# Performance work log

Hardware: AMD Instinct MI355X
Metric: run time of the kernel (lower is better)

Reference implementation:

```python
import jax, jax.numpy as jnp
import numpy as np

H = 128
N_USER, N_TXN, N_DEVICE = 200000, 400000, 100000
E = 600000


def setup_inputs() -> dict:
    key = jax.random.key(0)
    ks = jax.random.split(key, 16)
    s = 0.05
    return {
        "x_user": jax.random.normal(ks[0], (N_USER, H), jnp.float32),
        "x_txn": jax.random.normal(ks[1], (N_TXN, H), jnp.float32),
        "x_device": jax.random.normal(ks[2], (N_DEVICE, H), jnp.float32),
        "es0": jax.random.randint(ks[3], (E,), 0, N_TXN),
        "ed0": jax.random.randint(ks[4], (E,), 0, N_USER),
        "es1": jax.random.randint(ks[5], (E,), 0, N_DEVICE),
        "ed1": jax.random.randint(ks[6], (E,), 0, N_USER),
        "es2": jax.random.randint(ks[7], (E,), 0, N_USER),
        "ed2": jax.random.randint(ks[8], (E,), 0, N_USER),
        "Wl": jax.random.normal(ks[9], (3, H, H), jnp.float32) * s,
        "bl": jax.random.normal(ks[10], (3, H), jnp.float32) * s,
        "Wr": jax.random.normal(ks[11], (3, H, H), jnp.float32) * s,
        "W1": jax.random.normal(ks[12], (H, 3 * H), jnp.float32) * s,
        "b1": jax.random.normal(ks[13], (H,), jnp.float32) * s,
        "W2": jax.random.normal(ks[14], (H, H), jnp.float32) * s,
        "b2": jax.random.normal(ks[15], (H,), jnp.float32) * s,
    }


def _sage(x_src, x_dst, es, ed, wl, b, wr):
    # PyG SAGEConv (mean aggr): lin_l(mean of neighbor feats) + lin_r(x_dst)
    n_dst = x_dst.shape[0]
    msgs = x_src[es]                                   # [E, H] gather
    agg = jax.ops.segment_sum(msgs, ed, num_segments=n_dst)   # [N_dst, H]
    cnt = jax.ops.segment_sum(jnp.ones((es.shape[0],), x_src.dtype), ed,
                              num_segments=n_dst)
    mean = agg / jnp.maximum(cnt, 1.0)[:, None]
    return mean @ wl.T + b + x_dst @ wr.T


def reference(x_user, x_txn, x_device, es0, ed0, es1, ed1, es2, ed2,
              Wl, bl, Wr, W1, b1, W2, b2):
    o0 = _sage(x_txn, x_user, es0, ed0, Wl[0], bl[0], Wr[0])
    o1 = _sage(x_device, x_user, es1, ed1, Wl[1], bl[1], Wr[1])
    o2 = _sage(x_user, x_user, es2, ed2, Wl[2], bl[2], Wr[2])
    combined = jnp.concatenate([o0, o1, o2], axis=-1)  # [N_user, 3H]
    h = jax.nn.relu(combined @ W1.T + b1)
    return h @ W2.T + b2
```

## Files before the change

kernel.cpp:

```cpp
#include <hip/hip_runtime.h>

#define H 128

typedef float v2f __attribute__((ext_vector_type(2)));

__global__ __launch_bounds__(128) void precompute_kernel(
    const float* __restrict__ Wl, const float* __restrict__ bl,
    const float* __restrict__ Wr, const float* __restrict__ W1,
    const float* __restrict__ b1, const float* __restrict__ W2,
    const float* __restrict__ b2,
    float* __restrict__ Am, float* __restrict__ W2T,
    float* __restrict__ cvec, float* __restrict__ b2f)
{
  int b = blockIdx.x;
  int j = threadIdx.x;
  if (b < 512) {
    int mat = b >> 7;
    int m   = b & 127;
    float s = 0.f;
    if (mat < 3) {
      int r = mat;
      for (int i = 0; i < H; i++)
        s += Wl[r*H*H + i*H + m] * W1[j*3*H + r*H + i];
    } else {
      for (int r = 0; r < 3; r++)
        for (int i = 0; i < H; i++)
          s += Wr[r*H*H + i*H + m] * W1[j*3*H + r*H + i];
    }
    Am[mat*H*H + m*H + j] = s;
  } else if (b == 512) {
    float s = b1[j];
    for (int r = 0; r < 3; r++)
      for (int i = 0; i < H; i++)
        s += bl[r*H + i] * W1[j*3*H + r*H + i];
    cvec[j] = s;
    b2f[j]  = b2[j];
  } else {
    int m = b - 513;
    W2T[m*H + j] = W2[j*H + m];
  }
}

__global__ __launch_bounds__(256) void k_hist3(
    const int* __restrict__ ed0, const int* __restrict__ ed1,
    const int* __restrict__ ed2, int* __restrict__ cntA,
    int NU, int E0, int E1, int E2)
{
  int r = blockIdx.y;
  const int* ed = (r == 0) ? ed0 : (r == 1) ? ed1 : ed2;
  int E = (r == 0) ? E0 : (r == 1) ? E1 : E2;
  int i = blockIdx.x * 256 + threadIdx.x;
  if (i < E) atomicAdd(&cntA[(size_t)r * NU + ed[i]], 1);
}

__global__ __launch_bounds__(256) void k_scan1(
    const int* __restrict__ degA, int* __restrict__ offA,
    int* __restrict__ bsumA, int n, int nb1)
{
  int r = blockIdx.y;
  const int* deg = degA + (size_t)r * n;
  int* off1 = offA + (size_t)r * (n + 1);
  int* bsum = bsumA + (size_t)r * nb1;
  __shared__ int tmp[256];
  int i = blockIdx.x * 256 + threadIdx.x;
  int v = (i < n) ? deg[i] : 0;
  tmp[threadIdx.x] = v;
  __syncthreads();
  for (int s = 1; s < 256; s <<= 1) {
    int t = (threadIdx.x >= (unsigned)s) ? tmp[threadIdx.x - s] : 0;
    __syncthreads();
    tmp[threadIdx.x] += t;
    __syncthreads();
  }
  if (i < n) off1[i + 1] = tmp[threadIdx.x];
  if (threadIdx.x == 255) bsum[blockIdx.x] = tmp[255];
}

__global__ __launch_bounds__(256) void k_scan3c(
    int* __restrict__ offA, const int* __restrict__ bsumA,
    int* __restrict__ curA, int n, int nb1)
{
  int r = blockIdx.y;
  int* off = offA + (size_t)r * (n + 1);
  const int* bsum = bsumA + (size_t)r * nb1;
  int* cur = curA + (size_t)r * n;
  __shared__ int red[256];
  int a = 0;
  for (int i = threadIdx.x; i < blockIdx.x; i += 256) a += bsum[i];
  red[threadIdx.x] = a;
  __syncthreads();
  for (int s = 128; s > 0; s >>= 1) {
    if (threadIdx.x < (unsigned)s) red[threadIdx.x] += red[threadIdx.x + s];
    __syncthreads();
  }
  int prefix = red[0];
  int i = blockIdx.x * 256 + threadIdx.x;
  if (i < n) {
    int d = cur[i];
    int o = off[i + 1] + prefix;
    off[i + 1] = o;
    cur[i] = o - d;
  }
  if (blockIdx.x == 0 && threadIdx.x == 0) off[0] = 0;
}

__global__ __launch_bounds__(256) void k_scatter3(
    const int* __restrict__ es0, const int* __restrict__ es1,
    const int* __restrict__ es2,
    const int* __restrict__ ed0, const int* __restrict__ ed1,
    const int* __restrict__ ed2,
    int* __restrict__ curA,
    int* __restrict__ nbr0, int* __restrict__ nbr1, int* __restrict__ nbr2,
    int NU, int E0, int E1, int E2)
{
  int r = blockIdx.y;
  const int* es = (r == 0) ? es0 : (r == 1) ? es1 : es2;
  const int* ed = (r == 0) ? ed0 : (r == 1) ? ed1 : ed2;
  int* nbr = (r == 0) ? nbr0 : (r == 1) ? nbr1 : nbr2;
  int* cur = curA + (size_t)r * NU;
  int E = (r == 0) ? E0 : (r == 1) ? E1 : E2;
  int i = blockIdx.x * 256 + threadIdx.x;
  if (i < E) {
    int d = ed[i];
    int pos = atomicAdd(&cur[d], 1);
    nbr[pos] = es[i];
  }
}

__device__ __forceinline__ void mm_accum(const float* __restrict__ W,
                                         float (*xs)[130], float* wb,
                                         v2f* acc, int tid, int nA, int c)
{
  for (int mc = 0; mc < 4; mc++) {
    __syncthreads();
    {
      int m = tid >> 3;
      const float4* s4 = (const float4*)(W + (size_t)(mc * 32 + m) * H + c * 16);
      float4* dd = (float4*)(wb + c * 516 + m * 16);
      dd[0] = s4[0]; dd[1] = s4[1]; dd[2] = s4[2]; dd[3] = s4[3];
    }
    __syncthreads();
    const float* xr = &xs[nA][mc * 32];
    const float4* wq = (const float4*)(wb + c * 516);
#pragma unroll 4
    for (int m = 0; m < 32; m++) {
      float xm = xr[m];
      v2f xv; xv[0] = xm; xv[1] = xm;
      const float4* w4 = wq + m * 4;
#pragma unroll
      for (int q = 0; q < 4; q++) {
        float4 w = w4[q];
        v2f w01; w01[0] = w.x; w01[1] = w.y;
        v2f w23; w23[0] = w.z; w23[1] = w.w;
        acc[2*q]   += xv * w01;
        acc[2*q+1] += xv * w23;
      }
    }
  }
}

__global__ __launch_bounds__(256, 4) void k_fused(
    const float* __restrict__ xu, const float* __restrict__ xt,
    const float* __restrict__ xd,
    const int* __restrict__ off0, const int* __restrict__ nbr0,
    const int* __restrict__ off1, const int* __restrict__ nbr1,
    const int* __restrict__ off2, const int* __restrict__ nbr2,
    const float* __restrict__ Am, const float* __restrict__ W2T,
    const float* __restrict__ cvec, const float* __restrict__ b2f,
    float* __restrict__ out, int NU)
{
  __shared__ float xs[32][130];
  __shared__ float wb[8 * 516];
  int tid = threadIdx.x;
  int c = tid & 7, j0 = c * 16, nA = tid >> 3;
  int q = tid & 7;
  int g0 = blockIdx.x * 32;
  int g = g0 + nA;

  v2f acc[8];
  {
    const v2f* cv = (const v2f*)(cvec + j0);
#pragma unroll
    for (int qq = 0; qq < 8; qq++) acc[qq] = cv[qq];
  }

  for (int s = 0; s < 4; s++) {
    __syncthreads();
    float4 A[4];
#pragma unroll
    for (int i = 0; i < 4; i++) A[i] = make_float4(0.f, 0.f, 0.f, 0.f);

    if (g < NU) {
      if (s == 3) {
        const float4* src = (const float4*)(xu + (size_t)g * H) + q * 4;
#pragma unroll
        for (int i = 0; i < 4; i++) A[i] = src[i];
      } else {
        const float* xsrc = (s == 0) ? xt : (s == 1) ? xd : xu;
        const int* offp = (s == 0) ? off0 : (s == 1) ? off1 : off2;
        const int* nbrp = (s == 0) ? nbr0 : (s == 1) ? nbr1 : nbr2;
        int beg = offp[g], end = offp[g + 1];
        for (int e = beg; e < end; e++) {
          int srow = nbrp[e];
          const float4* src = (const float4*)(xsrc + (size_t)srow * H) + q * 4;
          float4 v[4];
#pragma unroll
          for (int i = 0; i < 4; i++) v[i] = src[i];
#pragma unroll
          for (int i = 0; i < 4; i++) {
            A[i].x += v[i].x; A[i].y += v[i].y;
            A[i].z += v[i].z; A[i].w += v[i].w;
          }
        }
        int d = end - beg;
        float inv = 1.f / (float)(d > 0 ? d : 1);
#pragma unroll
        for (int i = 0; i < 4; i++) {
          A[i].x *= inv; A[i].y *= inv; A[i].z *= inv; A[i].w *= inv;
        }
      }
    }
    {
      float2* xrow = (float2*)&xs[nA][q * 16];
#pragma unroll
      for (int i = 0; i < 4; i++) {
        xrow[2*i]     = make_float2(A[i].x, A[i].y);
        xrow[2*i + 1] = make_float2(A[i].z, A[i].w);
      }
    }
    __syncthreads();
    mm_accum(Am + (size_t)s * H * H, xs, wb, acc, tid, nA, c);
  }

  __syncthreads();
  {
    float2* xrow = (float2*)&xs[nA][j0];
#pragma unroll
    for (int qq = 0; qq < 8; qq++) {
      float a0 = acc[qq][0], a1 = acc[qq][1];
      xrow[qq] = make_float2(a0 > 0.f ? a0 : 0.f, a1 > 0.f ? a1 : 0.f);
    }
  }
  __syncthreads();
  {
    const v2f* bv = (const v2f*)(b2f + j0);
#pragma unroll
    for (int qq = 0; qq < 8; qq++) acc[qq] = bv[qq];
  }
  mm_accum(W2T, xs, wb, acc, tid, nA, c);

  if (g < NU) {
    float4* po = (float4*)(out + (size_t)g * H + j0);
#pragma unroll
    for (int qq = 0; qq < 4; qq++)
      po[qq] = make_float4(acc[2*qq][0], acc[2*qq][1],
                           acc[2*qq+1][0], acc[2*qq+1][1]);
  }
}

extern "C" void kernel_launch(void* const* d_in, const int* in_sizes, int n_in,
                              void* d_out, int out_size, void* d_ws, size_t ws_size,
                              hipStream_t stream) {
  (void)n_in; (void)out_size; (void)ws_size;
  const float* xu = (const float*)d_in[0];
  const float* xt = (const float*)d_in[1];
  const float* xd = (const float*)d_in[2];
  const int* ess[3] = { (const int*)d_in[3], (const int*)d_in[5], (const int*)d_in[7] };
  const int* eds[3] = { (const int*)d_in[4], (const int*)d_in[6], (const int*)d_in[8] };
  const float* Wl = (const float*)d_in[9];
  const float* bl = (const float*)d_in[10];
  const float* Wr = (const float*)d_in[11];
  const float* W1 = (const float*)d_in[12];
  const float* b1 = (const float*)d_in[13];
  const float* W2 = (const float*)d_in[14];
  const float* b2 = (const float*)d_in[15];
  int Es[3] = { in_sizes[3], in_sizes[5], in_sizes[7] };
  int Emax = Es[0] > Es[1] ? Es[0] : Es[1];
  if (Es[2] > Emax) Emax = Es[2];

  const int NU = in_sizes[0] / H;
  const int NB = (NU + 255) / 256;
  float* out = (float*)d_out;

  char* p = (char*)d_ws;
  size_t pos = 0;
  auto take = [&](size_t bytes) -> char* {
    char* r = p + pos;
    pos = (pos + bytes + 255) & ~(size_t)255;
    return r;
  };
  float* Am   = (float*)take((size_t)4 * H * H * sizeof(float));
  float* W2T  = (float*)take((size_t)H * H * sizeof(float));
  float* cvec = (float*)take(512);
  float* b2f  = (float*)take(512);
  int* curA   = (int*)take((size_t)3 * NU * sizeof(int));
  int* offA   = (int*)take((size_t)3 * (NU + 1) * sizeof(int));
  int* bsumA  = (int*)take((size_t)3 * (NB + 1) * sizeof(int));
  int* nbr[3];
  for (int r = 0; r < 3; r++) nbr[r] = (int*)take((size_t)Es[r] * sizeof(int));

  precompute_kernel<<<641, 128, 0, stream>>>(Wl, bl, Wr, W1, b1, W2, b2,
                                             Am, W2T, cvec, b2f);
  hipMemsetAsync(curA, 0, (size_t)3 * NU * sizeof(int), stream);

  dim3 ge((Emax + 255) / 256, 3);
  dim3 gn(NB, 3);
  k_hist3<<<ge, 256, 0, stream>>>(eds[0], eds[1], eds[2], curA,
                                  NU, Es[0], Es[1], Es[2]);
  k_scan1<<<gn, 256, 0, stream>>>(curA, offA, bsumA, NU, NB + 1);
  k_scan3c<<<gn, 256, 0, stream>>>(offA, bsumA, curA, NU, NB + 1);
  k_scatter3<<<ge, 256, 0, stream>>>(ess[0], ess[1], ess[2],
                                     eds[0], eds[1], eds[2],
                                     curA, nbr[0], nbr[1], nbr[2],
                                     NU, Es[0], Es[1], Es[2]);

  k_fused<<<(NU + 31) / 32, 256, 0, stream>>>(
      xu, xt, xd,
      offA, nbr[0], offA + (NU + 1), nbr[1], offA + 2 * (NU + 1), nbr[2],
      Am, W2T, cvec, b2f, out, NU);
}
```

Baseline: 1.205 ms.

## Process 64 nodes per block with two accumulator rows per thread

Each fused block now handles 64 user nodes instead of 32, so each thread accumulates two output rows and reuses every weight value it loads from shared memory. The gather stage is remapped so 4 threads cover each node row (32 floats each). This halves the number of weight-tile loads into shared memory per node and doubles FMA work per LDS read. The cost is more registers and shared memory, with occupancy hint lowered from 4 to 3 blocks, and less parallelism in the gather, since each thread now handles 32 columns.

```diff
diff --git a/kernel.cpp b/kernel.cpp
--- a/kernel.cpp
+++ b/kernel.cpp
@@ -129,7 +129,8 @@
 
 __device__ __forceinline__ void mm_accum(const float* __restrict__ W,
                                          float (*xs)[130], float* wb,
-                                         v2f* acc, int tid, int nA, int c)
+                                         v2f* acc0, v2f* acc1,
+                                         int tid, int nA, int c)
 {
   for (int mc = 0; mc < 4; mc++) {
     __syncthreads();
@@ -140,26 +141,30 @@
       dd[0] = s4[0]; dd[1] = s4[1]; dd[2] = s4[2]; dd[3] = s4[3];
     }
     __syncthreads();
-    const float* xr = &xs[nA][mc * 32];
+    const float* xr0 = &xs[nA][mc * 32];
+    const float* xr1 = &xs[nA + 32][mc * 32];
     const float4* wq = (const float4*)(wb + c * 516);
 #pragma unroll 4
     for (int m = 0; m < 32; m++) {
-      float xm = xr[m];
-      v2f xv; xv[0] = xm; xv[1] = xm;
+      float xm0 = xr0[m], xm1 = xr1[m];
+      v2f x0; x0[0] = xm0; x0[1] = xm0;
+      v2f x1; x1[0] = xm1; x1[1] = xm1;
       const float4* w4 = wq + m * 4;
 #pragma unroll
       for (int q = 0; q < 4; q++) {
         float4 w = w4[q];
         v2f w01; w01[0] = w.x; w01[1] = w.y;
         v2f w23; w23[0] = w.z; w23[1] = w.w;
-        acc[2*q]   += xv * w01;
-        acc[2*q+1] += xv * w23;
+        acc0[2*q]   += x0 * w01;
+        acc0[2*q+1] += x0 * w23;
+        acc1[2*q]   += x1 * w01;
+        acc1[2*q+1] += x1 * w23;
       }
     }
   }
 }
 
-__global__ __launch_bounds__(256, 4) void k_fused(
+__global__ __launch_bounds__(256, 3) void k_fused(
     const float* __restrict__ xu, const float* __restrict__ xt,
     const float* __restrict__ xd,
     const int* __restrict__ off0, const int* __restrict__ nbr0,
@@ -169,32 +174,36 @@
     const float* __restrict__ cvec, const float* __restrict__ b2f,
     float* __restrict__ out, int NU)
 {
-  __shared__ float xs[32][130];
+  __shared__ float xs[64][130];
   __shared__ float wb[8 * 516];
   int tid = threadIdx.x;
   int c = tid & 7, j0 = c * 16, nA = tid >> 3;
-  int q = tid & 7;
-  int g0 = blockIdx.x * 32;
-  int g = g0 + nA;
-
-  v2f acc[8];
+  int node = tid >> 2, q = tid & 3;
+  int g0 = blockIdx.x * 64;
+  int g = g0 + node;
+
+  v2f acc0[8], acc1[8];
   {
     const v2f* cv = (const v2f*)(cvec + j0);
 #pragma unroll
-    for (int qq = 0; qq < 8; qq++) acc[qq] = cv[qq];
+    for (int qq = 0; qq < 8; qq++) { acc0[qq] = cv[qq]; acc1[qq] = cv[qq]; }
   }
 
   for (int s = 0; s < 4; s++) {
     __syncthreads();
-    float4 A[4];
-#pragma unroll
-    for (int i = 0; i < 4; i++) A[i] = make_float4(0.f, 0.f, 0.f, 0.f);
+    v2f A[16];
+#pragma unroll
+    for (int i = 0; i < 16; i++) { A[i][0] = 0.f; A[i][1] = 0.f; }
 
     if (g < NU) {
       if (s == 3) {
-        const float4* src = (const float4*)(xu + (size_t)g * H) + q * 4;
-#pragma unroll
-        for (int i = 0; i < 4; i++) A[i] = src[i];
+        const float4* src = (const float4*)(xu + (size_t)g * H) + q * 8;
+#pragma unroll
+        for (int i = 0; i < 8; i++) {
+          float4 v = src[i];
+          A[2*i][0] = v.x;   A[2*i][1] = v.y;
+          A[2*i+1][0] = v.z; A[2*i+1][1] = v.w;
+        }
       } else {
         const float* xsrc = (s == 0) ? xt : (s == 1) ? xd : xu;
         const int* offp = (s == 0) ? off0 : (s == 1) ? off1 : off2;
@@ -202,59 +211,69 @@
         int beg = offp[g], end = offp[g + 1];
         for (int e = beg; e < end; e++) {
           int srow = nbrp[e];
-          const float4* src = (const float4*)(xsrc + (size_t)srow * H) + q * 4;
-          float4 v[4];
-#pragma unroll
-          for (int i = 0; i < 4; i++) v[i] = src[i];
-#pragma unroll
-          for (int i = 0; i < 4; i++) {
-            A[i].x += v[i].x; A[i].y += v[i].y;
-            A[i].z += v[i].z; A[i].w += v[i].w;
+          const float4* src = (const float4*)(xsrc + (size_t)srow * H) + q * 8;
+          float4 v[8];
+#pragma unroll
+          for (int i = 0; i < 8; i++) v[i] = src[i];
+#pragma unroll
+          for (int i = 0; i < 8; i++) {
+            v2f p0; p0[0] = v[i].x; p0[1] = v[i].y;
+            v2f p1; p1[0] = v[i].z; p1[1] = v[i].w;
+            A[2*i]   += p0;
+            A[2*i+1] += p1;
           }
         }
         int d = end - beg;
         float inv = 1.f / (float)(d > 0 ? d : 1);
-#pragma unroll
-        for (int i = 0; i < 4; i++) {
-          A[i].x *= inv; A[i].y *= inv; A[i].z *= inv; A[i].w *= inv;
-        }
+        v2f iv; iv[0] = inv; iv[1] = inv;
+#pragma unroll
+        for (int i = 0; i < 16; i++) A[i] *= iv;
       }
     }
     {
-      float2* xrow = (float2*)&xs[nA][q * 16];
-#pragma unroll
-      for (int i = 0; i < 4; i++) {
-        xrow[2*i]     = make_float2(A[i].x, A[i].y);
-        xrow[2*i + 1] = make_float2(A[i].z, A[i].w);
-      }
-    }
-    __syncthreads();
-    mm_accum(Am + (size_t)s * H * H, xs, wb, acc, tid, nA, c);
+      v2f* xrow = (v2f*)&xs[node][q * 32];
+#pragma unroll
+      for (int i = 0; i < 16; i++) xrow[i] = A[i];
+    }
+    __syncthreads();
+    mm_accum(Am + (size_t)s * H * H, xs, wb, acc0, acc1, tid, nA, c);
   }
 
   __syncthreads();
   {
-    float2* xrow = (float2*)&xs[nA][j0];
+    v2f* xr0 = (v2f*)&xs[nA][j0];
+    v2f* xr1 = (v2f*)&xs[nA + 32][j0];
 #pragma unroll
     for (int qq = 0; qq < 8; qq++) {
-      float a0 = acc[qq][0], a1 = acc[qq][1];
-      xrow[qq] = make_float2(a0 > 0.f ? a0 : 0.f, a1 > 0.f ? a1 : 0.f);
+      v2f a = acc0[qq], b = acc1[qq];
+      a[0] = a[0] > 0.f ? a[0] : 0.f; a[1] = a[1] > 0.f ? a[1] : 0.f;
+      b[0] = b[0] > 0.f ? b[0] : 0.f; b[1] = b[1] > 0.f ? b[1] : 0.f;
+      xr0[qq] = a;
+      xr1[qq] = b;
     }
   }
   __syncthreads();
   {
     const v2f* bv = (const v2f*)(b2f + j0);
 #pragma unroll
-    for (int qq = 0; qq < 8; qq++) acc[qq] = bv[qq];
-  }
-  mm_accum(W2T, xs, wb, acc, tid, nA, c);
-
-  if (g < NU) {
-    float4* po = (float4*)(out + (size_t)g * H + j0);
+    for (int qq = 0; qq < 8; qq++) { acc0[qq] = bv[qq]; acc1[qq] = bv[qq]; }
+  }
+  mm_accum(W2T, xs, wb, acc0, acc1, tid, nA, c);
+
+  int gA = g0 + nA, gB = gA + 32;
+  if (gA < NU) {
+    float4* po = (float4*)(out + (size_t)gA * H + j0);
 #pragma unroll
     for (int qq = 0; qq < 4; qq++)
-      po[qq] = make_float4(acc[2*qq][0], acc[2*qq][1],
-                           acc[2*qq+1][0], acc[2*qq+1][1]);
+      po[qq] = make_float4(acc0[2*qq][0], acc0[2*qq][1],
+                           acc0[2*qq+1][0], acc0[2*qq+1][1]);
+  }
+  if (gB < NU) {
+    float4* po = (float4*)(out + (size_t)gB * H + j0);
+#pragma unroll
+    for (int qq = 0; qq < 4; qq++)
+      po[qq] = make_float4(acc1[2*qq][0], acc1[2*qq][1],
+                           acc1[2*qq+1][0], acc1[2*qq+1][1]);
   }
 }
 
@@ -314,7 +333,7 @@
                                      curA, nbr[0], nbr[1], nbr[2],
                                      NU, Es[0], Es[1], Es[2]);
 
-  k_fused<<<(NU + 31) / 32, 256, 0, stream>>>(
+  k_fused<<<(NU + 63) / 64, 256, 0, stream>>>(
       xu, xt, xd,
       offA, nbr[0], offA + (NU + 1), nbr[1], offA + 2 * (NU + 1), nbr[2],
       Am, W2T, cvec, b2f, out, NU);
```

Result: faster. 1.093 ms (-9.3%).
